# Optimization experiments

Hardware: AMD Instinct MI355X
Metric: run time of the kernel (lower is better)

The kernel has to match this reference:

```python
import jax, jax.numpy as jnp
import numpy as np

B, T, H, NH, L, V, FF = 2, 1024, 1024, 16, 6, 8192, 4096
D = H // NH
EPS = 1e-5


def _ln(x, g, b):
    mu = jnp.mean(x, axis=-1, keepdims=True)
    var = jnp.mean(jnp.square(x - mu), axis=-1, keepdims=True)
    return (x - mu) * jax.lax.rsqrt(var + EPS) * g + b


def setup_inputs() -> dict:
    key = jax.random.key(0)
    ks = jax.random.split(key, 12)
    s = 1.0 / np.sqrt(H)
    return {
        "x": jax.random.randint(ks[0], (B, T), 0, V),
        "tok_emb": jax.random.normal(ks[1], (V, H), jnp.float32) * s,
        "pos_emb": jax.random.normal(ks[2], (1, T, H), jnp.float32) * s,
        "Wq": jax.random.normal(ks[3], (L, H, H), jnp.float32) * s,
        "bq": jnp.zeros((L, H), jnp.float32),
        "Wk": jax.random.normal(ks[4], (L, H, H), jnp.float32) * s,
        "bk": jnp.zeros((L, H), jnp.float32),
        "Wv": jax.random.normal(ks[5], (L, H, H), jnp.float32) * s,
        "bv": jnp.zeros((L, H), jnp.float32),
        "Wo": jax.random.normal(ks[6], (L, H, H), jnp.float32) * s,
        "bo": jnp.zeros((L, H), jnp.float32),
        "W1": jax.random.normal(ks[7], (L, H, FF), jnp.float32) * s,
        "b1": jnp.zeros((L, FF), jnp.float32),
        "W2": jax.random.normal(ks[8], (L, FF, H), jnp.float32) * (1.0 / np.sqrt(FF)),
        "b2": jnp.zeros((L, H), jnp.float32),
        "ln1_g": jnp.ones((L, H), jnp.float32),
        "ln1_b": jnp.zeros((L, H), jnp.float32),
        "ln2_g": jnp.ones((L, H), jnp.float32),
        "ln2_b": jnp.zeros((L, H), jnp.float32),
        "lnf_g": jnp.ones((H,), jnp.float32),
        "lnf_b": jnp.zeros((H,), jnp.float32),
        "headW": jax.random.normal(ks[9], (H, V), jnp.float32) * s,
        "headb": jnp.zeros((V,), jnp.float32),
    }


def _transformer(x, tok_emb, pos_emb, Wq, bq, Wk, bk, Wv, bv, Wo, bo,
                 W1, b1, W2, b2, ln1_g, ln1_b, ln2_g, ln2_b, lnf_g, lnf_b,
                 headW, headb):
    Tcur = x.shape[1]
    h = tok_emb[x] + pos_emb[:, :Tcur, :]            # [B,T,H]
    mask = jnp.tril(jnp.ones((Tcur, Tcur), bool))    # causal [T,T]
    scale = 1.0 / np.sqrt(D)

    def block(h, p):
        (wq, q_b, wk, k_b, wv, v_b, wo, o_b,
         w1, b1_, w2, b2_, g1, be1, g2, be2) = p
        q = (h @ wq + q_b).reshape(B, Tcur, NH, D)
        k = (h @ wk + k_b).reshape(B, Tcur, NH, D)
        v = (h @ wv + v_b).reshape(B, Tcur, NH, D)
        att = jnp.einsum('bqnd,bknd->bnqk', q, k) * scale
        att = jnp.where(mask, att, -jnp.inf)
        w = jax.nn.softmax(att, axis=-1)
        o = jnp.einsum('bnqk,bknd->bqnd', w, v).reshape(B, Tcur, H)
        h = _ln(h + (o @ wo + o_b), g1, be1)          # post-LN after attention
        m = jax.nn.gelu(h @ w1 + b1_, approximate=False) @ w2 + b2_
        h = _ln(h + m, g2, be2)                       # post-LN after MLP
        return h, None

    params = (Wq, bq, Wk, bk, Wv, bv, Wo, bo, W1, b1, W2, b2,
              ln1_g, ln1_b, ln2_g, ln2_b)
    h, _ = jax.lax.scan(block, h, params)
    h = _ln(h, lnf_g, lnf_b)
    return h @ headW + headb                          # [B,T,V]


def reference(x, tok_emb, pos_emb, Wq, bq, Wk, bk, Wv, bv, Wo, bo,
              W1, b1, W2, b2, ln1_g, ln1_b, ln2_g, ln2_b, lnf_g, lnf_b,
              headW, headb):
    return _transformer(x, tok_emb, pos_emb, Wq, bq, Wk, bk, Wv, bv, Wo, bo,
                        W1, b1, W2, b2, ln1_g, ln1_b, ln2_g, ln2_b,
                        lnf_g, lnf_b, headW, headb)
```

## Files before the change

kernel.cpp:

```cpp
#include <hip/hip_runtime.h>
#include <hip/hip_bf16.h>

#define DEV __device__ __forceinline__

typedef unsigned short u16;
typedef __attribute__((ext_vector_type(8))) short bf16x8;
typedef __attribute__((ext_vector_type(4))) float f32x4;

static constexpr int MB_ = 2;
static constexpr int T_  = 1024;
static constexpr int H_  = 1024;
static constexpr int NH_ = 16;
static constexpr int L_  = 6;
static constexpr int V_  = 8192;
static constexpr int FF_ = 4096;
static constexpr int M_  = MB_ * T_;
static constexpr int QKVN = 3 * H_;

DEV u16 f2bf(float x) {
  __hip_bfloat16 h = __float2bfloat16(x);
  return *reinterpret_cast<u16*>(&h);
}

__global__ __launch_bounds__(256) void embed_kernel(
    const int* __restrict__ x, const float* __restrict__ tok,
    const float* __restrict__ pos, float* __restrict__ h, u16* __restrict__ hb)
{
  int i = blockIdx.x;
  int t = threadIdx.x;
  int id = x[i];
  int tt = i & (T_ - 1);
  float4 a = *(const float4*)(tok + (size_t)id * H_ + t * 4);
  float4 b = *(const float4*)(pos + (size_t)tt * H_ + t * 4);
  float4 r = make_float4(a.x + b.x, a.y + b.y, a.z + b.z, a.w + b.w);
  *(float4*)(h + (size_t)i * H_ + t * 4) = r;
  ushort4 u = make_ushort4(f2bf(r.x), f2bf(r.y), f2bf(r.z), f2bf(r.w));
  *(ushort4*)(hb + (size_t)i * H_ + t * 4) = u;
}

DEV void transpose_tile(const float* __restrict__ W, u16* __restrict__ WT, int R, int C)
{
  __shared__ float Ts[64][65];
  int bx = blockIdx.x, by = blockIdx.y;
  if (bx * 64 >= C || by * 64 >= R) return;
  int r0 = by * 64, c0 = bx * 64;
  int t = threadIdx.x;
  int lr = t >> 4;
  int lcq = (t & 15) * 4;
  #pragma unroll
  for (int it = 0; it < 4; ++it) {
    int r = it * 16 + lr;
    float4 v = *(const float4*)(W + (size_t)(r0 + r) * C + c0 + lcq);
    Ts[r][lcq + 0] = v.x; Ts[r][lcq + 1] = v.y;
    Ts[r][lcq + 2] = v.z; Ts[r][lcq + 3] = v.w;
  }
  __syncthreads();
  #pragma unroll
  for (int it = 0; it < 4; ++it) {
    int n = it * 16 + lr;
    ushort4 u = make_ushort4(f2bf(Ts[lcq + 0][n]), f2bf(Ts[lcq + 1][n]),
                             f2bf(Ts[lcq + 2][n]), f2bf(Ts[lcq + 3][n]));
    *(ushort4*)(WT + (size_t)(c0 + n) * R + r0 + lcq) = u;
  }
}

__global__ __launch_bounds__(256) void transpose_one(
    const float* __restrict__ W, u16* __restrict__ WT, int R, int C)
{ transpose_tile(W, WT, R, C); }

__global__ __launch_bounds__(256) void transpose_layer6(
    const float* __restrict__ Wq, const float* __restrict__ Wk,
    const float* __restrict__ Wv, const float* __restrict__ Wo,
    const float* __restrict__ W1, const float* __restrict__ W2,
    u16* qT, u16* kT, u16* vT, u16* oT, u16* w1T, u16* w2T)
{
  int z = blockIdx.z;
  const float* W; u16* WT; int R, C;
  switch (z) {
    case 0: W = Wq; WT = qT;  R = H_;  C = H_;  break;
    case 1: W = Wk; WT = kT;  R = H_;  C = H_;  break;
    case 2: W = Wv; WT = vT;  R = H_;  C = H_;  break;
    case 3: W = Wo; WT = oT;  R = H_;  C = H_;  break;
    case 4: W = W1; WT = w1T; R = H_;  C = FF_; break;
    default:W = W2; WT = w2T; R = FF_; C = H_;  break;
  }
  transpose_tile(W, WT, R, C);
}

__global__ __launch_bounds__(256) void concat_qkv_bias(
    const float* __restrict__ bq, const float* __restrict__ bk,
    const float* __restrict__ bv, float* __restrict__ outb)
{
  int l = blockIdx.x;
  for (int j = threadIdx.x; j < H_; j += 256) {
    outb[(size_t)l * QKVN + j]          = bq[(size_t)l * H_ + j];
    outb[(size_t)l * QKVN + H_ + j]     = bk[(size_t)l * H_ + j];
    outb[(size_t)l * QKVN + 2 * H_ + j] = bv[(size_t)l * H_ + j];
  }
}


#define GLOAD_LDS16(g, l)                                              \
  __builtin_amdgcn_global_load_lds(                                    \
      (const __attribute__((address_space(1))) void*)(g),              \
      (__attribute__((address_space(3))) void*)(l), 16, 0, 0)

DEV void stage_t(const u16* __restrict__ G, int ldk, int r0g, int kofs,
                 u16* lds, int w, int lane)
{
  const int rr = lane >> 2;
  #pragma unroll
  for (int j = 0; j < 2; ++j) {
    const int row0 = w * 32 + j * 16;
    const int row = row0 + rr;
    const int c = (lane & 3) ^ (row & 3);
    const u16* g = G + (size_t)(r0g + row) * ldk + kofs + c * 8;
    GLOAD_LDS16(g, lds + row0 * 32);
  }
}

DEV bf16x8 frag3(const u16* lds, int rr, int ch) {
  return *(const bf16x8*)(lds + rr * 32 + ((ch ^ (rr & 3)) * 8));
}

template<int N>
DEV void wait_vm_barrier() {
  asm volatile("s_waitcnt vmcnt(%0)" :: "n"(N) : "memory");
  __builtin_amdgcn_s_barrier();
}

DEV void comp3(const u16* As, const u16* Bs, f32x4 (&acc)[4][4],
               int wr, int wc, int lc, int lg)
{
  bf16x8 af[4], bv[4];
  #pragma unroll
  for (int mi = 0; mi < 4; ++mi)
    af[mi] = frag3(As, wr * 64 + mi * 16 + lc, lg);
  #pragma unroll
  for (int ni = 0; ni < 4; ++ni)
    bv[ni] = frag3(Bs, wc * 64 + ni * 16 + lc, lg);
  #pragma unroll
  for (int mi = 0; mi < 4; ++mi)
    #pragma unroll
    for (int ni = 0; ni < 4; ++ni)
      acc[mi][ni] = __builtin_amdgcn_mfma_f32_16x16x32_bf16(af[mi], bv[ni], acc[mi][ni], 0, 0, 0);
}

template<bool PARTIAL, bool DO_GELU, bool WF, bool WB>
__global__ __launch_bounds__(256, 2) void gemm3(
    const u16* __restrict__ A, const u16* __restrict__ BT,
    const float* __restrict__ bias, float* __restrict__ Cf,
    u16* __restrict__ Cb, float* __restrict__ P, int N, int K, int Ksub)
{
  __shared__ __align__(16) u16 As[4][128][32];
  __shared__ __align__(16) u16 Bs[4][128][32];

  const int tid = threadIdx.x;
  const int lane = tid & 63, w = tid >> 6;
  const int wr = w >> 1, wc = w & 1;
  const int lc = lane & 15, lg = lane >> 4;
  const int m0 = blockIdx.y * 128, n0 = blockIdx.x * 128;
  const int kb = blockIdx.z * Ksub;
  const int NT = Ksub >> 5;

  f32x4 acc[4][4];
  #pragma unroll
  for (int i = 0; i < 4; ++i)
    #pragma unroll
    for (int j = 0; j < 4; ++j) {
      f32x4 z = {0.f, 0.f, 0.f, 0.f};
      acc[i][j] = z;
    }

  auto STG = [&](int t, int b) {
    stage_t(A,  K, m0, kb + t * 32, &As[b][0][0], w, lane);
    stage_t(BT, K, n0, kb + t * 32, &Bs[b][0][0], w, lane);
  };

  STG(0, 0);
  STG(1, 1);
  int t = 0;
  for (; t < NT - 2; ++t) {
    STG(t + 2, (t + 2) & 3);
    wait_vm_barrier<8>();
    comp3(&As[t & 3][0][0], &Bs[t & 3][0][0], acc, wr, wc, lc, lg);
  }
  wait_vm_barrier<4>();
  comp3(&As[t & 3][0][0], &Bs[t & 3][0][0], acc, wr, wc, lc, lg);
  ++t;
  wait_vm_barrier<0>();
  comp3(&As[t & 3][0][0], &Bs[t & 3][0][0], acc, wr, wc, lc, lg);

  const size_t zofs = (size_t)blockIdx.z * M_ * N;
  #pragma unroll
  for (int mi = 0; mi < 4; ++mi) {
    #pragma unroll
    for (int ni = 0; ni < 4; ++ni) {
      int gn = n0 + wc * 64 + ni * 16 + lc;
      float bvv = PARTIAL ? 0.f : bias[gn];
      #pragma unroll
      for (int r = 0; r < 4; ++r) {
        int gm = m0 + wr * 64 + mi * 16 + lg * 4 + r;
        float v = acc[mi][ni][r];
        if (PARTIAL) {
          P[zofs + (size_t)gm * N + gn] = v;
        } else {
          v += bvv;
          if (DO_GELU) v = 0.5f * v * (1.f + erff(v * 0.70710678118654752f));
          if (WF) Cf[(size_t)gm * N + gn] = v;
          if (WB) Cb[(size_t)gm * N + gn] = f2bf(v);
        }
      }
    }
  }
}

__global__ __launch_bounds__(256) void ln_kernel(
    const float* __restrict__ X,
    const float* __restrict__ g, const float* __restrict__ be,
    u16* __restrict__ Hb)
{
  __shared__ float red[8];
  int row = blockIdx.x, t = threadIdx.x;
  int lane = t & 63, w = t >> 6;
  float4 v = *(const float4*)(X + (size_t)row * H_ + t * 4);
  float s = v.x + v.y + v.z + v.w;
  float q = v.x * v.x + v.y * v.y + v.z * v.z + v.w * v.w;
  #pragma unroll
  for (int o = 1; o < 64; o <<= 1) { s += __shfl_xor(s, o); q += __shfl_xor(q, o); }
  if (lane == 0) { red[w] = s; red[4 + w] = q; }
  __syncthreads();
  float S = red[0] + red[1] + red[2] + red[3];
  float Q = red[4] + red[5] + red[6] + red[7];
  float mu  = S * (1.f / H_);
  float var = Q * (1.f / H_) - mu * mu;
  float inv = rsqrtf(var + 1e-5f);
  float4 gv = *(const float4*)(g  + t * 4);
  float4 bv = *(const float4*)(be + t * 4);
  ushort4 u = make_ushort4(f2bf((v.x - mu) * inv * gv.x + bv.x),
                           f2bf((v.y - mu) * inv * gv.y + bv.y),
                           f2bf((v.z - mu) * inv * gv.z + bv.z),
                           f2bf((v.w - mu) * inv * gv.w + bv.w));
  *(ushort4*)(Hb + (size_t)row * H_ + t * 4) = u;
}

__global__ __launch_bounds__(256) void ln2_kernel(
    const float* __restrict__ P, int S,
    const float* __restrict__ bias,
    const float* __restrict__ g, const float* __restrict__ be,
    float* __restrict__ h, u16* __restrict__ hb)
{
  __shared__ float red[8];
  int row = blockIdx.x, t = threadIdx.x;
  int lane = t & 63, w = t >> 6;
  float4 v = *(const float4*)(h + (size_t)row * H_ + t * 4);
  float4 bb = *(const float4*)(bias + t * 4);
  v.x += bb.x; v.y += bb.y; v.z += bb.z; v.w += bb.w;
  for (int s0 = 0; s0 < S; ++s0) {
    float4 p = *(const float4*)(P + (size_t)s0 * M_ * H_ + (size_t)row * H_ + t * 4);
    v.x += p.x; v.y += p.y; v.z += p.z; v.w += p.w;
  }
  float s = v.x + v.y + v.z + v.w;
  float q = v.x * v.x + v.y * v.y + v.z * v.z + v.w * v.w;
  #pragma unroll
  for (int o = 1; o < 64; o <<= 1) { s += __shfl_xor(s, o); q += __shfl_xor(q, o); }
  if (lane == 0) { red[w] = s; red[4 + w] = q; }
  __syncthreads();
  float S1 = red[0] + red[1] + red[2] + red[3];
  float Q1 = red[4] + red[5] + red[6] + red[7];
  float mu  = S1 * (1.f / H_);
  float var = Q1 * (1.f / H_) - mu * mu;
  float inv = rsqrtf(var + 1e-5f);
  float4 gv = *(const float4*)(g  + t * 4);
  float4 bv = *(const float4*)(be + t * 4);
  float o0 = (v.x - mu) * inv * gv.x + bv.x;
  float o1 = (v.y - mu) * inv * gv.y + bv.y;
  float o2 = (v.z - mu) * inv * gv.z + bv.z;
  float o3 = (v.w - mu) * inv * gv.w + bv.w;
  *(float4*)(h + (size_t)row * H_ + t * 4) = make_float4(o0, o1, o2, o3);
  ushort4 u = make_ushort4(f2bf(o0), f2bf(o1), f2bf(o2), f2bf(o3));
  *(ushort4*)(hb + (size_t)row * H_ + t * 4) = u;
}

__global__ __launch_bounds__(256) void attn_kernel(
    const u16* __restrict__ qkv, u16* __restrict__ Og)
{
  __shared__ __align__(16) u16 Qs[64][72];
  __shared__ __align__(16) u16 Ks[64][72];
  __shared__ __align__(16) u16 Vs[64][72];
  __shared__ __align__(16) u16 Ps[4][16][72];

  const int qb = blockIdx.x;
  const int bh = blockIdx.y;
  const int b = bh >> 4, hh = bh & 15;
  const int q0 = qb * 64;
  const size_t base  = ((size_t)b * T_) * QKVN + (size_t)hh * 64;
  const size_t baseO = ((size_t)b * T_) * H_ + (size_t)hh * 64;

  const int tid = threadIdx.x;
  const int lane = tid & 63, w = tid >> 6;
  const int lc = lane & 15, lg = lane >> 4;

  {
    int r = tid >> 3, d = (tid & 7) << 3;
    #pragma unroll
    for (int i = 0; i < 2; ++i)
      *(bf16x8*)&Qs[i * 32 + r][d] =
        *(const bf16x8*)(qkv + base + (size_t)(q0 + i * 32 + r) * QKVN + d);
  }
  __syncthreads();
  bf16x8 aq0 = *(const bf16x8*)&Qs[w * 16 + lc][lg * 8];
  bf16x8 aq1 = *(const bf16x8*)&Qs[w * 16 + lc][32 + lg * 8];

  float m_r[4], l_r[4];
  f32x4 oa[4];
  #pragma unroll
  for (int i = 0; i < 4; ++i) {
    m_r[i] = -1e30f; l_r[i] = 0.f;
    f32x4 z = {0.f, 0.f, 0.f, 0.f};
    oa[i] = z;
  }
  const float sc2 = 0.125f * 1.4426950408889634f;

  for (int kv = 0; kv <= qb; ++kv) {
    __syncthreads();
    {
      int r = tid >> 3, d = (tid & 7) << 3;
      #pragma unroll
      for (int i = 0; i < 2; ++i)
        *(bf16x8*)&Ks[i * 32 + r][d] =
          *(const bf16x8*)(qkv + base + H_ + (size_t)(kv * 64 + i * 32 + r) * QKVN + d);
      int vk = tid & 31, vd = ((tid >> 5) << 3);
      #pragma unroll
      for (int i = 0; i < 2; ++i) {
        bf16x8 vv = *(const bf16x8*)(qkv + base + 2 * H_ + (size_t)(kv * 64 + i * 32 + vk) * QKVN + vd);
        #pragma unroll
        for (int j = 0; j < 8; ++j) Vs[vd + j][i * 32 + vk] = ((const u16*)&vv)[j];
      }
    }
    __syncthreads();

    f32x4 sfr[4];
    #pragma unroll
    for (int ni = 0; ni < 4; ++ni) { f32x4 z = {0.f,0.f,0.f,0.f}; sfr[ni] = z; }
    #pragma unroll
    for (int ni = 0; ni < 4; ++ni) {
      bf16x8 bk0 = *(const bf16x8*)&Ks[ni * 16 + lc][lg * 8];
      bf16x8 bk1 = *(const bf16x8*)&Ks[ni * 16 + lc][32 + lg * 8];
      sfr[ni] = __builtin_amdgcn_mfma_f32_16x16x32_bf16(aq0, bk0, sfr[ni], 0, 0, 0);
      sfr[ni] = __builtin_amdgcn_mfma_f32_16x16x32_bf16(aq1, bk1, sfr[ni], 0, 0, 0);
    }
    if (kv == qb) {
      #pragma unroll
      for (int ni = 0; ni < 4; ++ni)
        #pragma unroll
        for (int r = 0; r < 4; ++r)
          if (ni * 16 + lc > w * 16 + lg * 4 + r) sfr[ni][r] = -1e30f;
    }
    #pragma unroll
    for (int r = 0; r < 4; ++r) {
      float pm = fmaxf(fmaxf(sfr[0][r], sfr[1][r]), fmaxf(sfr[2][r], sfr[3][r]));
      pm = fmaxf(pm, __shfl_xor(pm, 1));
      pm = fmaxf(pm, __shfl_xor(pm, 2));
      pm = fmaxf(pm, __shfl_xor(pm, 4));
      pm = fmaxf(pm, __shfl_xor(pm, 8));
      float mn = fmaxf(m_r[r], pm);
      float al = exp2f(sc2 * (m_r[r] - mn));
      m_r[r] = mn; l_r[r] *= al;
      #pragma unroll
      for (int f = 0; f < 4; ++f) oa[f][r] *= al;
      float rs = 0.f;
      #pragma unroll
      for (int ni = 0; ni < 4; ++ni) {
        float p = exp2f(sc2 * (sfr[ni][r] - mn));
        sfr[ni][r] = p; rs += p;
      }
      rs += __shfl_xor(rs, 1); rs += __shfl_xor(rs, 2);
      rs += __shfl_xor(rs, 4); rs += __shfl_xor(rs, 8);
      l_r[r] += rs;
    }
    #pragma unroll
    for (int ni = 0; ni < 4; ++ni)
      #pragma unroll
      for (int r = 0; r < 4; ++r)
        Ps[w][lg * 4 + r][ni * 16 + lc] = f2bf(sfr[ni][r]);
    bf16x8 ap0 = *(const bf16x8*)&Ps[w][lc][lg * 8];
    bf16x8 ap1 = *(const bf16x8*)&Ps[w][lc][32 + lg * 8];
    #pragma unroll
    for (int f = 0; f < 4; ++f) {
      bf16x8 bv0 = *(const bf16x8*)&Vs[f * 16 + lc][lg * 8];
      bf16x8 bv1 = *(const bf16x8*)&Vs[f * 16 + lc][32 + lg * 8];
      oa[f] = __builtin_amdgcn_mfma_f32_16x16x32_bf16(ap0, bv0, oa[f], 0, 0, 0);
      oa[f] = __builtin_amdgcn_mfma_f32_16x16x32_bf16(ap1, bv1, oa[f], 0, 0, 0);
    }
  }

  #pragma unroll
  for (int r = 0; r < 4; ++r) {
    float inv = 1.f / l_r[r];
    int grow = q0 + w * 16 + lg * 4 + r;
    #pragma unroll
    for (int f = 0; f < 4; ++f)
      Og[baseO + (size_t)grow * H_ + f * 16 + lc] = f2bf(oa[f][r] * inv);
  }
}

extern "C" void kernel_launch(void* const* d_in, const int* in_sizes, int n_in,
                              void* d_out, int out_size, void* d_ws, size_t ws_size,
                              hipStream_t stream)
{
  const int*   x    = (const int*)  d_in[0];
  const float* tok  = (const float*)d_in[1];
  const float* pos  = (const float*)d_in[2];
  const float* Wq   = (const float*)d_in[3];
  const float* bq   = (const float*)d_in[4];
  const float* Wk   = (const float*)d_in[5];
  const float* bk   = (const float*)d_in[6];
  const float* Wv   = (const float*)d_in[7];
  const float* bv   = (const float*)d_in[8];
  const float* Wo   = (const float*)d_in[9];
  const float* bo   = (const float*)d_in[10];
  const float* W1   = (const float*)d_in[11];
  const float* b1   = (const float*)d_in[12];
  const float* W2   = (const float*)d_in[13];
  const float* b2   = (const float*)d_in[14];
  const float* g1   = (const float*)d_in[15];
  const float* be1  = (const float*)d_in[16];
  const float* g2   = (const float*)d_in[17];
  const float* be2  = (const float*)d_in[18];
  const float* gf   = (const float*)d_in[19];
  const float* bef  = (const float*)d_in[20];
  const float* hW   = (const float*)d_in[21];
  const float* hbias= (const float*)d_in[22];
  float* out = (float*)d_out;

  char* wsp = (char*)d_ws;
  size_t off = 0;
  auto alloc = [&](size_t bytes) -> void* {
    void* p = wsp + off;
    off += (bytes + 255) & ~(size_t)255;
    return p;
  };
  float* h    = (float*)alloc((size_t)M_ * H_ * 4);
  u16*   hb   = (u16*)  alloc((size_t)M_ * H_ * 2);
  u16*   qkv  = (u16*)  alloc((size_t)M_ * QKVN * 2);
  u16*   ob_  = (u16*)  alloc((size_t)M_ * H_ * 2);
  u16*   m1   = (u16*)  alloc((size_t)M_ * FF_ * 2);
  float* P    = (float*)alloc((size_t)4 * M_ * H_ * 4);
  u16*   hT   = (u16*)P;
  size_t hTbytes = (size_t)V_ * H_ * 2;
  (void)hTbytes;
  u16*   qkvT = (u16*)  alloc((size_t)QKVN * H_ * 2);
  u16*   oT   = (u16*)  alloc((size_t)H_ * H_ * 2);
  u16*   w1T  = (u16*)  alloc((size_t)H_ * FF_ * 2);
  u16*   w2T  = (u16*)  alloc((size_t)FF_ * H_ * 2);
  float* bqkv = (float*)alloc((size_t)L_ * QKVN * 4);
  (void)in_sizes; (void)n_in; (void)out_size; (void)ws_size;

  embed_kernel<<<M_, 256, 0, stream>>>(x, tok, pos, h, hb);
  concat_qkv_bias<<<L_, 256, 0, stream>>>(bq, bk, bv, bqkv);

  for (int l = 0; l < L_; ++l) {
    transpose_layer6<<<dim3(64, 64, 6), 256, 0, stream>>>(
        Wq + (size_t)l * H_ * H_, Wk + (size_t)l * H_ * H_,
        Wv + (size_t)l * H_ * H_, Wo + (size_t)l * H_ * H_,
        W1 + (size_t)l * H_ * FF_, W2 + (size_t)l * FF_ * H_,
        qkvT, qkvT + (size_t)H_ * H_, qkvT + 2 * (size_t)H_ * H_,
        oT, w1T, w2T);
    gemm3<false, false, false, true><<<dim3(QKVN / 128, M_ / 128, 1), 256, 0, stream>>>(
        hb, qkvT, bqkv + (size_t)l * QKVN, nullptr, qkv, nullptr, QKVN, H_, H_);
    attn_kernel<<<dim3(T_ / 64, MB_ * NH_), 256, 0, stream>>>(qkv, ob_);
    gemm3<true, false, false, false><<<dim3(H_ / 128, M_ / 128, 2), 256, 0, stream>>>(
        ob_, oT, nullptr, nullptr, nullptr, P, H_, H_, H_ / 2);
    ln2_kernel<<<M_, 256, 0, stream>>>(P, 2, bo + l * H_, g1 + l * H_, be1 + l * H_, h, hb);
    gemm3<false, true, false, true><<<dim3(FF_ / 128, M_ / 128, 1), 256, 0, stream>>>(
        hb, w1T, b1 + (size_t)l * FF_, nullptr, m1, nullptr, FF_, H_, H_);
    gemm3<true, false, false, false><<<dim3(H_ / 128, M_ / 128, 4), 256, 0, stream>>>(
        m1, w2T, nullptr, nullptr, nullptr, P, H_, FF_, FF_ / 4);
    ln2_kernel<<<M_, 256, 0, stream>>>(P, 4, b2 + l * H_, g2 + l * H_, be2 + l * H_, h, hb);
  }

  ln_kernel<<<M_, 256, 0, stream>>>(h, gf, bef, hb);
  transpose_one<<<dim3(V_ / 64, H_ / 64), 256, 0, stream>>>(hW, hT, H_, V_);
  gemm3<false, false, true, false><<<dim3(V_ / 128, M_ / 128, 1), 256, 0, stream>>>(
      hb, hT, hbias, out, nullptr, nullptr, V_, H_, H_);
}
```

Before: 1.141 ms.

## Switch GEMMs to double-buffered LDS, 4 blocks/CU, and BN=96 QKV tiles

```diff
diff --git a/kernel.cpp b/kernel.cpp
--- a/kernel.cpp
+++ b/kernel.cpp
@@ -105,17 +105,20 @@
       (const __attribute__((address_space(1))) void*)(g),              \
       (__attribute__((address_space(3))) void*)(l), 16, 0, 0)
 
-DEV void stage_t(const u16* __restrict__ G, int ldk, int r0g, int kofs,
-                 u16* lds, int w, int lane)
+template<int ROWS>
+DEV void stage_rows(const u16* __restrict__ G, int ldk, int r0g, int kofs,
+                    u16* lds, int w, int lane)
 {
   const int rr = lane >> 2;
-  #pragma unroll
-  for (int j = 0; j < 2; ++j) {
-    const int row0 = w * 32 + j * 16;
-    const int row = row0 + rr;
-    const int c = (lane & 3) ^ (row & 3);
-    const u16* g = G + (size_t)(r0g + row) * ldk + kofs + c * 8;
-    GLOAD_LDS16(g, lds + row0 * 32);
+  if (ROWS == 128 || w < ROWS / 32) {
+    #pragma unroll
+    for (int j = 0; j < 2; ++j) {
+      const int row0 = w * 32 + j * 16;
+      const int row = row0 + rr;
+      const int c = (lane & 3) ^ (row & 3);
+      const u16* g = G + (size_t)(r0g + row) * ldk + kofs + c * 8;
+      GLOAD_LDS16(g, lds + row0 * 32);
+    }
   }
 }
 
@@ -123,80 +126,70 @@
   return *(const bf16x8*)(lds + rr * 32 + ((ch ^ (rr & 3)) * 8));
 }
 
-template<int N>
-DEV void wait_vm_barrier() {
-  asm volatile("s_waitcnt vmcnt(%0)" :: "n"(N) : "memory");
-  __builtin_amdgcn_s_barrier();
-}
-
-DEV void comp3(const u16* As, const u16* Bs, f32x4 (&acc)[4][4],
+template<int NFN>
+DEV void comp4(const u16* As, const u16* Bs, f32x4 (&acc)[4][NFN],
                int wr, int wc, int lc, int lg)
 {
-  bf16x8 af[4], bv[4];
+  bf16x8 af[4], bv[NFN];
   #pragma unroll
   for (int mi = 0; mi < 4; ++mi)
     af[mi] = frag3(As, wr * 64 + mi * 16 + lc, lg);
   #pragma unroll
-  for (int ni = 0; ni < 4; ++ni)
-    bv[ni] = frag3(Bs, wc * 64 + ni * 16 + lc, lg);
+  for (int ni = 0; ni < NFN; ++ni)
+    bv[ni] = frag3(Bs, wc * (NFN * 16) + ni * 16 + lc, lg);
   #pragma unroll
   for (int mi = 0; mi < 4; ++mi)
     #pragma unroll
-    for (int ni = 0; ni < 4; ++ni)
+    for (int ni = 0; ni < NFN; ++ni)
       acc[mi][ni] = __builtin_amdgcn_mfma_f32_16x16x32_bf16(af[mi], bv[ni], acc[mi][ni], 0, 0, 0);
 }
 
-template<bool PARTIAL, bool DO_GELU, bool WF, bool WB>
-__global__ __launch_bounds__(256, 2) void gemm3(
+template<int BN, bool PARTIAL, bool DO_GELU, bool WF, bool WB>
+__global__ __launch_bounds__(256, 4) void gemm4(
     const u16* __restrict__ A, const u16* __restrict__ BT,
     const float* __restrict__ bias, float* __restrict__ Cf,
     u16* __restrict__ Cb, float* __restrict__ P, int N, int K, int Ksub)
 {
-  __shared__ __align__(16) u16 As[4][128][32];
-  __shared__ __align__(16) u16 Bs[4][128][32];
+  constexpr int NFN = BN / 32;
+  __shared__ __align__(16) u16 As[2][128][32];
+  __shared__ __align__(16) u16 Bs[2][BN][32];
 
   const int tid = threadIdx.x;
   const int lane = tid & 63, w = tid >> 6;
   const int wr = w >> 1, wc = w & 1;
   const int lc = lane & 15, lg = lane >> 4;
-  const int m0 = blockIdx.y * 128, n0 = blockIdx.x * 128;
+  const int m0 = blockIdx.y * 128, n0 = blockIdx.x * BN;
   const int kb = blockIdx.z * Ksub;
   const int NT = Ksub >> 5;
 
-  f32x4 acc[4][4];
+  f32x4 acc[4][NFN];
   #pragma unroll
   for (int i = 0; i < 4; ++i)
     #pragma unroll
-    for (int j = 0; j < 4; ++j) {
+    for (int j = 0; j < NFN; ++j) {
       f32x4 z = {0.f, 0.f, 0.f, 0.f};
       acc[i][j] = z;
     }
 
   auto STG = [&](int t, int b) {
-    stage_t(A,  K, m0, kb + t * 32, &As[b][0][0], w, lane);
-    stage_t(BT, K, n0, kb + t * 32, &Bs[b][0][0], w, lane);
+    stage_rows<128>(A,  K, m0, kb + t * 32, &As[b][0][0], w, lane);
+    stage_rows<BN >(BT, K, n0, kb + t * 32, &Bs[b][0][0], w, lane);
   };
 
   STG(0, 0);
-  STG(1, 1);
-  int t = 0;
-  for (; t < NT - 2; ++t) {
-    STG(t + 2, (t + 2) & 3);
-    wait_vm_barrier<8>();
-    comp3(&As[t & 3][0][0], &Bs[t & 3][0][0], acc, wr, wc, lc, lg);
-  }
-  wait_vm_barrier<4>();
-  comp3(&As[t & 3][0][0], &Bs[t & 3][0][0], acc, wr, wc, lc, lg);
-  ++t;
-  wait_vm_barrier<0>();
-  comp3(&As[t & 3][0][0], &Bs[t & 3][0][0], acc, wr, wc, lc, lg);
+  for (int t = 0; t < NT; ++t) {
+    asm volatile("s_waitcnt vmcnt(0)" ::: "memory");
+    __builtin_amdgcn_s_barrier();
+    if (t + 1 < NT) STG(t + 1, (t + 1) & 1);
+    comp4<NFN>(&As[t & 1][0][0], &Bs[t & 1][0][0], acc, wr, wc, lc, lg);
+  }
 
   const size_t zofs = (size_t)blockIdx.z * M_ * N;
   #pragma unroll
   for (int mi = 0; mi < 4; ++mi) {
     #pragma unroll
-    for (int ni = 0; ni < 4; ++ni) {
-      int gn = n0 + wc * 64 + ni * 16 + lc;
+    for (int ni = 0; ni < NFN; ++ni) {
+      int gn = n0 + wc * (NFN * 16) + ni * 16 + lc;
       float bvv = PARTIAL ? 0.f : bias[gn];
       #pragma unroll
       for (int r = 0; r < 4; ++r) {
@@ -448,8 +441,6 @@
   u16*   m1   = (u16*)  alloc((size_t)M_ * FF_ * 2);
   float* P    = (float*)alloc((size_t)4 * M_ * H_ * 4);
   u16*   hT   = (u16*)P;
-  size_t hTbytes = (size_t)V_ * H_ * 2;
-  (void)hTbytes;
   u16*   qkvT = (u16*)  alloc((size_t)QKVN * H_ * 2);
   u16*   oT   = (u16*)  alloc((size_t)H_ * H_ * 2);
   u16*   w1T  = (u16*)  alloc((size_t)H_ * FF_ * 2);
@@ -467,21 +458,21 @@
         W1 + (size_t)l * H_ * FF_, W2 + (size_t)l * FF_ * H_,
         qkvT, qkvT + (size_t)H_ * H_, qkvT + 2 * (size_t)H_ * H_,
         oT, w1T, w2T);
-    gemm3<false, false, false, true><<<dim3(QKVN / 128, M_ / 128, 1), 256, 0, stream>>>(
+    gemm4<96, false, false, false, true><<<dim3(QKVN / 96, M_ / 128, 1), 256, 0, stream>>>(
         hb, qkvT, bqkv + (size_t)l * QKVN, nullptr, qkv, nullptr, QKVN, H_, H_);
     attn_kernel<<<dim3(T_ / 64, MB_ * NH_), 256, 0, stream>>>(qkv, ob_);
-    gemm3<true, false, false, false><<<dim3(H_ / 128, M_ / 128, 2), 256, 0, stream>>>(
-        ob_, oT, nullptr, nullptr, nullptr, P, H_, H_, H_ / 2);
-    ln2_kernel<<<M_, 256, 0, stream>>>(P, 2, bo + l * H_, g1 + l * H_, be1 + l * H_, h, hb);
-    gemm3<false, true, false, true><<<dim3(FF_ / 128, M_ / 128, 1), 256, 0, stream>>>(
+    gemm4<128, true, false, false, false><<<dim3(H_ / 128, M_ / 128, 4), 256, 0, stream>>>(
+        ob_, oT, nullptr, nullptr, nullptr, P, H_, H_, H_ / 4);
+    ln2_kernel<<<M_, 256, 0, stream>>>(P, 4, bo + l * H_, g1 + l * H_, be1 + l * H_, h, hb);
+    gemm4<128, false, true, false, true><<<dim3(FF_ / 128, M_ / 128, 1), 256, 0, stream>>>(
         hb, w1T, b1 + (size_t)l * FF_, nullptr, m1, nullptr, FF_, H_, H_);
-    gemm3<true, false, false, false><<<dim3(H_ / 128, M_ / 128, 4), 256, 0, stream>>>(
+    gemm4<128, true, false, false, false><<<dim3(H_ / 128, M_ / 128, 4), 256, 0, stream>>>(
         m1, w2T, nullptr, nullptr, nullptr, P, H_, FF_, FF_ / 4);
     ln2_kernel<<<M_, 256, 0, stream>>>(P, 4, b2 + l * H_, g2 + l * H_, be2 + l * H_, h, hb);
   }
 
   ln_kernel<<<M_, 256, 0, stream>>>(h, gf, bef, hb);
   transpose_one<<<dim3(V_ / 64, H_ / 64), 256, 0, stream>>>(hW, hT, H_, V_);
-  gemm3<false, false, true, false><<<dim3(V_ / 128, M_ / 128, 1), 256, 0, stream>>>(
+  gemm4<128, false, false, true, false><<<dim3(V_ / 128, M_ / 128, 1), 256, 0, stream>>>(
       hb, hT, hbias, out, nullptr, nullptr, V_, H_, H_);
 }
```

Result: slower. 1.174 ms (+2.9%).
